# Kernel optimization log

Measured on AMD Instinct MI355X. Metric: run time of the kernel, lower is better.

The kernel has to match this reference:

```python
import jax, jax.numpy as jnp
import numpy as np

DIM = 256
HEADS = 8
GH = GW = 8
NTOK = GH * GW            # 64 tokens per window
NW = 49                   # windows per image (56x56 / 8x8)
BATCH = 64
B_ = BATCH * NW           # 3136
POS_DIM = (DIM // 4) // 4 # 16, DynamicPosBias pos_dim
LBIAS = (2 * GH - 1) * (2 * GW - 1)  # 225 relative offsets
EPS = 1e-5


def _ln(x, g, b):
    m = jnp.mean(x, axis=-1, keepdims=True)
    v = jnp.mean((x - m) ** 2, axis=-1, keepdims=True)
    return (x - m) * jax.lax.rsqrt(v + EPS) * g + b


def _make_buffers():
    # biases: all relative (dh, dw) offsets, shape (LBIAS, 2) float
    h = np.arange(1 - GH, GH)
    w = np.arange(1 - GW, GW)
    biases = np.stack(np.meshgrid(h, w, indexing='ij')).reshape(2, -1).T.astype(np.float32)
    # relative_position_index: (NTOK, NTOK) int32 in [0, LBIAS)
    coords = np.stack(np.meshgrid(np.arange(GH), np.arange(GW), indexing='ij')).reshape(2, -1)
    rel = coords[:, :, None] - coords[:, None, :]
    rel = rel.transpose(1, 2, 0).astype(np.int64)
    rel[..., 0] += GH - 1
    rel[..., 1] += GW - 1
    rel[..., 0] *= 2 * GW - 1
    idx = rel.sum(-1).astype(np.int32)
    return jnp.asarray(biases), jnp.asarray(idx)


def setup_inputs() -> dict:
    key = jax.random.key(0)
    ks = iter(jax.random.split(key, 32))
    def w(shape, s=0.02):
        return jax.random.normal(next(ks), shape, jnp.float32) * s
    biases, rel_idx = _make_buffers()
    return {
        'x': jax.random.normal(next(ks), (B_, NTOK, DIM), jnp.float32),
        'mask': jnp.zeros((NW, NTOK, NTOK), jnp.float32),
        'qkv_w': w((3 * DIM, DIM)), 'qkv_b': jnp.zeros((3 * DIM,), jnp.float32),
        'proj_w': w((DIM, DIM)), 'proj_b': jnp.zeros((DIM,), jnp.float32),
        'pos_proj_w': w((POS_DIM, 2)), 'pos_proj_b': jnp.zeros((POS_DIM,), jnp.float32),
        'ln1_g': jnp.ones((POS_DIM,), jnp.float32), 'ln1_b': jnp.zeros((POS_DIM,), jnp.float32),
        'fc1_w': w((POS_DIM, POS_DIM)), 'fc1_b': jnp.zeros((POS_DIM,), jnp.float32),
        'ln2_g': jnp.ones((POS_DIM,), jnp.float32), 'ln2_b': jnp.zeros((POS_DIM,), jnp.float32),
        'fc2_w': w((POS_DIM, POS_DIM)), 'fc2_b': jnp.zeros((POS_DIM,), jnp.float32),
        'ln3_g': jnp.ones((POS_DIM,), jnp.float32), 'ln3_b': jnp.zeros((POS_DIM,), jnp.float32),
        'fc3_w': w((HEADS, POS_DIM)), 'fc3_b': jnp.zeros((HEADS,), jnp.float32),
        'biases': biases, 'rel_idx': rel_idx,
    }


def _forward(x, mask, qkv_w, qkv_b, proj_w, proj_b,
             pos_proj_w, pos_proj_b, ln1_g, ln1_b, fc1_w, fc1_b,
             ln2_g, ln2_b, fc2_w, fc2_b, ln3_g, ln3_b, fc3_w, fc3_b,
             biases, rel_idx):
    Bw, N, C = x.shape
    hd = C // HEADS
    scale = hd ** -0.5
    qkv = (x @ qkv_w.T + qkv_b).reshape(Bw, N, 3, HEADS, hd)
    qkv = jnp.transpose(qkv, (2, 0, 3, 1, 4))  # (3, B_, H, N, hd)
    q, k, v = qkv[0] * scale, qkv[1], qkv[2]
    attn = jnp.einsum('bhnd,bhmd->bhnm', q, k)  # (B_, H, N, N)
    # DynamicPosBias MLP (residual=False): pos3(pos2(pos1(pos_proj(biases))))
    p = biases @ pos_proj_w.T + pos_proj_b
    p = jax.nn.relu(_ln(p, ln1_g, ln1_b)) @ fc1_w.T + fc1_b
    p = jax.nn.relu(_ln(p, ln2_g, ln2_b)) @ fc2_w.T + fc2_b
    p = jax.nn.relu(_ln(p, ln3_g, ln3_b)) @ fc3_w.T + fc3_b  # (LBIAS, H)
    rpb = jnp.transpose(p[rel_idx], (2, 0, 1))  # gather -> (H, N, N)
    attn = attn + rpb[None]
    nW = mask.shape[0]
    attn = attn.reshape(Bw // nW, nW, HEADS, N, N) + mask[None, :, None]
    attn = jax.nn.softmax(attn.reshape(Bw, HEADS, N, N), axis=-1)
    out = jnp.einsum('bhnm,bhmd->bhnd', attn, v)
    out = jnp.transpose(out, (0, 2, 1, 3)).reshape(Bw, N, C)
    return out @ proj_w.T + proj_b


def reference(x, mask, qkv_w, qkv_b, proj_w, proj_b,
              pos_proj_w, pos_proj_b, ln1_g, ln1_b, fc1_w, fc1_b,
              ln2_g, ln2_b, fc2_w, fc2_b, ln3_g, ln3_b, fc3_w, fc3_b,
              biases, rel_idx):
    return _forward(x, mask, qkv_w, qkv_b, proj_w, proj_b,
                    pos_proj_w, pos_proj_b, ln1_g, ln1_b, fc1_w, fc1_b,
                    ln2_g, ln2_b, fc2_w, fc2_b, ln3_g, ln3_b, fc3_w, fc3_b,
                    biases, rel_idx)
```

## Files before the change

### kernel.cpp

```cpp
#include <hip/hip_runtime.h>

#define NTOKS 64
#define DIMS 256
#define NHEADS 8
#define HDIM 32
#define NWIN 49
#define NBLK 3136

typedef __bf16 bf16x8 __attribute__((ext_vector_type(8)));
typedef float f32x4 __attribute__((ext_vector_type(4)));

__device__ __forceinline__ unsigned short f2bf(float f) {
    union { float f; unsigned u; } c; c.f = f;
    unsigned u = c.u;
    u += 0x7fffu + ((u >> 16) & 1u);
    return (unsigned short)(u >> 16);
}

template<int NOUT>
__device__ __forceinline__ void ln_relu_fc(const float* v, const float* g, const float* bb,
                                           const float* fw, const float* fb, float* o) {
    float m = 0.f;
#pragma unroll
    for (int j = 0; j < 16; ++j) m += v[j];
    m *= (1.f / 16.f);
    float var = 0.f;
#pragma unroll
    for (int j = 0; j < 16; ++j) { float d = v[j] - m; var += d * d; }
    var *= (1.f / 16.f);
    float inv = rsqrtf(var + 1e-5f);
    float t[16];
#pragma unroll
    for (int j = 0; j < 16; ++j) {
        float xx = (v[j] - m) * inv * g[j] + bb[j];
        t[j] = xx > 0.f ? xx : 0.f;
    }
#pragma unroll
    for (int i = 0; i < NOUT; ++i) {
        float ss = fb[i];
#pragma unroll
        for (int j = 0; j < 16; ++j) ss += fw[i * 16 + j] * t[j];
        o[i] = ss;
    }
}

__global__ void prep_kernel(
    const float* __restrict__ qkv_w, const float* __restrict__ qkv_b,
    const float* __restrict__ proj_w, const float* __restrict__ mask,
    const float* __restrict__ pos_proj_w, const float* __restrict__ pos_proj_b,
    const float* __restrict__ ln1_g, const float* __restrict__ ln1_b,
    const float* __restrict__ fc1_w, const float* __restrict__ fc1_b,
    const float* __restrict__ ln2_g, const float* __restrict__ ln2_b,
    const float* __restrict__ fc2_w, const float* __restrict__ fc2_b,
    const float* __restrict__ ln3_g, const float* __restrict__ ln3_b,
    const float* __restrict__ fc3_w, const float* __restrict__ fc3_b,
    const float* __restrict__ biases, const int* __restrict__ rel_idx,
    unsigned short* __restrict__ qkvw_bf, unsigned short* __restrict__ projw_bf,
    float* __restrict__ qkvb_s, float* __restrict__ rpb_perm,
    float* __restrict__ mask_perm)
{
    const int tid = threadIdx.x;
    const int b = blockIdx.x;
    const float SC = 0.17677669529663687f;

    if (b == 0) {
        __shared__ float p_sh[225 * 8];
        if (tid < 225) {
            float bx = biases[2 * tid], by = biases[2 * tid + 1];
            float v[16], u[16];
#pragma unroll
            for (int j = 0; j < 16; ++j)
                v[j] = pos_proj_w[2 * j] * bx + pos_proj_w[2 * j + 1] * by + pos_proj_b[j];
            ln_relu_fc<16>(v, ln1_g, ln1_b, fc1_w, fc1_b, u);
            ln_relu_fc<16>(u, ln2_g, ln2_b, fc2_w, fc2_b, v);
            ln_relu_fc<8>(v, ln3_g, ln3_b, fc3_w, fc3_b, u);
#pragma unroll
            for (int h = 0; h < 8; ++h) p_sh[tid * 8 + h] = u[h];
        }
        __syncthreads();
        for (int e = tid; e < 32768; e += 256) {
            int nt = e & 3, l16 = (e >> 2) & 15, m = (e >> 6) & 63, h = e >> 12;
            rpb_perm[e] = p_sh[rel_idx[m * 64 + nt * 16 + l16] * 8 + h];
        }
    } else {
        const int t0 = (b - 1) * 256 + tid, NTH = 127 * 256;
        for (int e = t0; e < 196608; e += NTH) {
            int j = e & 7, lane = (e >> 3) & 63, kk = (e >> 9) & 7, tile = e >> 12;
            int src = (tile * 16 + (lane & 15)) * 256 + kk * 32 + (lane >> 4) * 8 + j;
            float f = qkv_w[src];
            if (src < 65536) f *= SC;
            qkvw_bf[e] = f2bf(f);
        }
        for (int e = t0; e < 65536; e += NTH) {
            int j = e & 7, lane = (e >> 3) & 63, kk = (e >> 9) & 7, tile = e >> 12;
            int src = (tile * 16 + (lane & 15)) * 256 + kk * 32 + (lane >> 4) * 8 + j;
            projw_bf[e] = f2bf(proj_w[src]);
        }
        for (int e = t0; e < 200704; e += NTH) {
            int nt = e & 3, l16 = (e >> 2) & 15, m = (e >> 6) & 63, w = e >> 12;
            mask_perm[e] = mask[w * 4096 + m * 64 + nt * 16 + l16];
        }
        if (b == 1) {
            for (int e = tid; e < 768; e += 256)
                qkvb_s[e] = qkv_b[e] * (e < 256 ? SC : 1.f);
        }
    }
}

#define XS_OFF 0
#define Q_OFF  16896
#define K_OFF  33792
#define VT_OFF 50688
#define LDS_TOT 69120
#define PS_OFF 0
#define CTX_OFF 0
#define FO_OFF 16896

__global__ __launch_bounds__(1024, 4) void attn_kernel(
    const float* __restrict__ x,
    const unsigned short* __restrict__ qkvw, const float* __restrict__ qkvb,
    const unsigned short* __restrict__ projw, const float* __restrict__ projb,
    const float* __restrict__ rpb_perm, const float* __restrict__ mask_perm,
    float* __restrict__ out)
{
    __shared__ __align__(16) unsigned short lds[LDS_TOT];
    const int tid  = threadIdx.x;
    const int wv   = tid >> 6;
    const int lane = tid & 63;
    const int quad = lane >> 4;
    const int l16  = lane & 15;
    const int blk  = blockIdx.x;
    const int w    = blk % NWIN;
    const f32x4 FZ = {0.f, 0.f, 0.f, 0.f};

    {
        const float4* xv = (const float4*)(x + (size_t)blk * (NTOKS * DIMS));
        for (int i = tid; i < NTOKS * DIMS / 4; i += 1024) {
            float4 f = xv[i];
            int row = i >> 6, c4 = (i & 63) << 2;
            ushort4 u;
            u.x = f2bf(f.x); u.y = f2bf(f.y); u.z = f2bf(f.z); u.w = f2bf(f.w);
            *(ushort4*)&lds[XS_OFF + row * 264 + c4] = u;
        }
    }
    __syncthreads();

    {
        f32x4 acc[4][3];
#pragma unroll
        for (int mt = 0; mt < 4; ++mt)
#pragma unroll
            for (int nt = 0; nt < 3; ++nt) acc[mt][nt] = FZ;
        const unsigned short* wq = qkvw + (size_t)(wv * 3) * 8 * 512;
        for (int kk = 0; kk < 8; ++kk) {
            bf16x8 a[4], bb[3];
#pragma unroll
            for (int mt = 0; mt < 4; ++mt)
                a[mt] = *(const bf16x8*)&lds[XS_OFF + (mt * 16 + l16) * 264 + kk * 32 + quad * 8];
#pragma unroll
            for (int nt = 0; nt < 3; ++nt)
                bb[nt] = *(const bf16x8*)&wq[(nt * 8 + kk) * 512 + lane * 8];
#pragma unroll
            for (int nt = 0; nt < 3; ++nt)
#pragma unroll
                for (int mt = 0; mt < 4; ++mt)
                    acc[mt][nt] = __builtin_amdgcn_mfma_f32_16x16x32_bf16(a[mt], bb[nt], acc[mt][nt], 0, 0, 0);
        }
#pragma unroll
        for (int nt = 0; nt < 3; ++nt) {
            int ob = wv * 48 + nt * 16;
            int o = ob + l16;
            float bias = qkvb[o];
            if (ob < 256) {
#pragma unroll
                for (int mt = 0; mt < 4; ++mt)
#pragma unroll
                    for (int r = 0; r < 4; ++r)
                        lds[Q_OFF + (mt * 16 + quad * 4 + r) * 264 + o] = f2bf(acc[mt][nt][r] + bias);
            } else if (ob < 512) {
                int oo = o - 256;
#pragma unroll
                for (int mt = 0; mt < 4; ++mt)
#pragma unroll
                    for (int r = 0; r < 4; ++r)
                        lds[K_OFF + (mt * 16 + quad * 4 + r) * 264 + oo] = f2bf(acc[mt][nt][r] + bias);
            } else {
                int oo = o - 512;
#pragma unroll
                for (int mt = 0; mt < 4; ++mt) {
                    ushort4 u;
                    u.x = f2bf(acc[mt][nt][0] + bias);
                    u.y = f2bf(acc[mt][nt][1] + bias);
                    u.z = f2bf(acc[mt][nt][2] + bias);
                    u.w = f2bf(acc[mt][nt][3] + bias);
                    *(ushort4*)&lds[VT_OFF + oo * 72 + mt * 16 + quad * 4] = u;
                }
            }
        }
    }
    __syncthreads();

    const int h  = wv >> 1;
    const int hf = wv & 1;
    f32x4 s[2][4];
    {
        bf16x8 aq[2], bk[4];
#pragma unroll
        for (int mt = 0; mt < 2; ++mt)
            aq[mt] = *(const bf16x8*)&lds[Q_OFF + (hf * 32 + mt * 16 + l16) * 264 + h * 32 + quad * 8];
#pragma unroll
        for (int nt = 0; nt < 4; ++nt)
            bk[nt] = *(const bf16x8*)&lds[K_OFF + (nt * 16 + l16) * 264 + h * 32 + quad * 8];
#pragma unroll
        for (int mt = 0; mt < 2; ++mt)
#pragma unroll
            for (int nt = 0; nt < 4; ++nt)
                s[mt][nt] = __builtin_amdgcn_mfma_f32_16x16x32_bf16(aq[mt], bk[nt], FZ, 0, 0, 0);
    }
    {
        const f32x4* rp4 = (const f32x4*)rpb_perm;
        const f32x4* mk4 = (const f32x4*)mask_perm;
#pragma unroll
        for (int mt = 0; mt < 2; ++mt)
#pragma unroll
            for (int r = 0; r < 4; ++r) {
                int m = hf * 32 + mt * 16 + quad * 4 + r;
                f32x4 rv = rp4[(h * 64 + m) * 16 + l16];
                f32x4 mv = mk4[(w * 64 + m) * 16 + l16];
#pragma unroll
                for (int nt = 0; nt < 4; ++nt)
                    s[mt][nt][r] += rv[nt] + mv[nt];
            }
    }
#pragma unroll
    for (int mt = 0; mt < 2; ++mt)
#pragma unroll
        for (int r = 0; r < 4; ++r) {
            float mx = fmaxf(fmaxf(s[mt][0][r], s[mt][1][r]), fmaxf(s[mt][2][r], s[mt][3][r]));
            mx = fmaxf(mx, __shfl_xor(mx, 1));
            mx = fmaxf(mx, __shfl_xor(mx, 2));
            mx = fmaxf(mx, __shfl_xor(mx, 4));
            mx = fmaxf(mx, __shfl_xor(mx, 8));
            float sum = 0.f;
#pragma unroll
            for (int nt = 0; nt < 4; ++nt) {
                float e = __expf(s[mt][nt][r] - mx);
                s[mt][nt][r] = e; sum += e;
            }
            sum += __shfl_xor(sum, 1);
            sum += __shfl_xor(sum, 2);
            sum += __shfl_xor(sum, 4);
            sum += __shfl_xor(sum, 8);
            float inv = 1.0f / sum;
#pragma unroll
            for (int nt = 0; nt < 4; ++nt) s[mt][nt][r] *= inv;
        }
    __syncthreads();

#pragma unroll
    for (int mt = 0; mt < 2; ++mt)
#pragma unroll
        for (int r = 0; r < 4; ++r) {
            int m = hf * 32 + mt * 16 + quad * 4 + r;
#pragma unroll
            for (int nt = 0; nt < 4; ++nt)
                lds[PS_OFF + h * 4608 + m * 72 + nt * 16 + l16] = f2bf(s[mt][nt][r]);
        }
    __syncthreads();

    f32x4 ov[2][2];
#pragma unroll
    for (int mt = 0; mt < 2; ++mt)
#pragma unroll
        for (int nt = 0; nt < 2; ++nt) ov[mt][nt] = FZ;
#pragma unroll
    for (int ks = 0; ks < 2; ++ks) {
        bf16x8 ap[2], bv[2];
#pragma unroll
        for (int mt = 0; mt < 2; ++mt)
            ap[mt] = *(const bf16x8*)&lds[PS_OFF + h * 4608 + (hf * 32 + mt * 16 + l16) * 72 + ks * 32 + quad * 8];
#pragma unroll
        for (int nt = 0; nt < 2; ++nt)
            bv[nt] = *(const bf16x8*)&lds[VT_OFF + (h * 32 + nt * 16 + l16) * 72 + ks * 32 + quad * 8];
#pragma unroll
        for (int mt = 0; mt < 2; ++mt)
#pragma unroll
            for (int nt = 0; nt < 2; ++nt)
                ov[mt][nt] = __builtin_amdgcn_mfma_f32_16x16x32_bf16(ap[mt], bv[nt], ov[mt][nt], 0, 0, 0);
    }
    __syncthreads();

#pragma unroll
    for (int mt = 0; mt < 2; ++mt)
#pragma unroll
        for (int r = 0; r < 4; ++r) {
            int t = hf * 32 + mt * 16 + quad * 4 + r;
#pragma unroll
            for (int nt = 0; nt < 2; ++nt)
                lds[CTX_OFF + t * 264 + h * 32 + nt * 16 + l16] = f2bf(ov[mt][nt][r]);
        }
    __syncthreads();

    {
        f32x4 accC[4];
#pragma unroll
        for (int mt = 0; mt < 4; ++mt) accC[mt] = FZ;
        const unsigned short* pw = projw + (size_t)wv * 8 * 512;
        for (int kk = 0; kk < 8; ++kk) {
            bf16x8 a[4];
#pragma unroll
            for (int mt = 0; mt < 4; ++mt)
                a[mt] = *(const bf16x8*)&lds[CTX_OFF + (mt * 16 + l16) * 264 + kk * 32 + quad * 8];
            bf16x8 bb = *(const bf16x8*)&pw[kk * 512 + lane * 8];
#pragma unroll
            for (int mt = 0; mt < 4; ++mt)
                accC[mt] = __builtin_amdgcn_mfma_f32_16x16x32_bf16(a[mt], bb, accC[mt], 0, 0, 0);
        }
        float* fo = (float*)&lds[FO_OFF];
        int o = wv * 16 + l16;
        float pb = projb[o];
#pragma unroll
        for (int mt = 0; mt < 4; ++mt)
#pragma unroll
            for (int r = 0; r < 4; ++r)
                fo[(mt * 16 + quad * 4 + r) * 260 + o] = accC[mt][r] + pb;
    }
    __syncthreads();
    {
        float* ob = out + (size_t)blk * (NTOKS * DIMS);
        const float* fo = (const float*)&lds[FO_OFF];
        for (int i = tid; i < NTOKS * DIMS / 4; i += 1024) {
            int row = i >> 6, c4 = (i & 63) << 2;
            float4 v = *(const float4*)&fo[row * 260 + c4];
            *(float4*)&ob[row * 256 + c4] = v;
        }
    }
}

extern "C" void kernel_launch(void* const* d_in, const int* in_sizes, int n_in,
                              void* d_out, int out_size, void* d_ws, size_t ws_size,
                              hipStream_t stream) {
    const float* x          = (const float*)d_in[0];
    const float* mask       = (const float*)d_in[1];
    const float* qkv_w      = (const float*)d_in[2];
    const float* qkv_b      = (const float*)d_in[3];
    const float* proj_w     = (const float*)d_in[4];
    const float* proj_b     = (const float*)d_in[5];
    const float* pos_proj_w = (const float*)d_in[6];
    const float* pos_proj_b = (const float*)d_in[7];
    const float* ln1_g      = (const float*)d_in[8];
    const float* ln1_b      = (const float*)d_in[9];
    const float* fc1_w      = (const float*)d_in[10];
    const float* fc1_b      = (const float*)d_in[11];
    const float* ln2_g      = (const float*)d_in[12];
    const float* ln2_b      = (const float*)d_in[13];
    const float* fc2_w      = (const float*)d_in[14];
    const float* fc2_b      = (const float*)d_in[15];
    const float* ln3_g      = (const float*)d_in[16];
    const float* ln3_b      = (const float*)d_in[17];
    const float* fc3_w      = (const float*)d_in[18];
    const float* fc3_b      = (const float*)d_in[19];
    const float* biases     = (const float*)d_in[20];
    const int*   rel_idx    = (const int*)d_in[21];
    float* out = (float*)d_out;

    char* ws = (char*)d_ws;
    unsigned short* qkvw_bf  = (unsigned short*)(ws);
    unsigned short* projw_bf = (unsigned short*)(ws + 393216);
    float* qkvb_s    = (float*)(ws + 524288);
    float* rpb_perm  = (float*)(ws + 528384);
    float* mask_perm = (float*)(ws + 659456);

    prep_kernel<<<dim3(128), dim3(256), 0, stream>>>(
        qkv_w, qkv_b, proj_w, mask, pos_proj_w, pos_proj_b,
        ln1_g, ln1_b, fc1_w, fc1_b, ln2_g, ln2_b, fc2_w, fc2_b,
        ln3_g, ln3_b, fc3_w, fc3_b, biases, rel_idx,
        qkvw_bf, projw_bf, qkvb_s, rpb_perm, mask_perm);

    attn_kernel<<<dim3(NBLK), dim3(1024), 0, stream>>>(
        x, qkvw_bf, qkvb_s, projw_bf, proj_b, rpb_perm, mask_perm, out);
}
```

Measured before the change: 604.8 us.

## Restructure attention to one wave per head with register-resident Q/K/V/P

The attention kernel is rebuilt so each of 8 waves owns one head. Each wave computes its own Q, K and V slices straight into MFMA register fragments (Q/K computed transposed), runs the scores, softmax and PV in registers, and only stages the context through an XOR-swizzled LDS buffer before the output projection. The output is written directly to global memory rather than through an LDS staging pass. The rpb/mask permutations in the prep kernel are changed to match the new transposed score layout. This removes several LDS round-trips and barriers and shrinks LDS use. In exchange, register pressure per wave rises, blocks are 512 threads, and the global stores are 4-byte scattered writes instead of float4.

```diff
diff --git a/kernel.cpp b/kernel.cpp
--- a/kernel.cpp
+++ b/kernel.cpp
@@ -3,11 +3,11 @@
 #define NTOKS 64
 #define DIMS 256
 #define NHEADS 8
-#define HDIM 32
 #define NWIN 49
 #define NBLK 3136
 
 typedef __bf16 bf16x8 __attribute__((ext_vector_type(8)));
+typedef __bf16 bf16x4 __attribute__((ext_vector_type(4)));
 typedef float f32x4 __attribute__((ext_vector_type(4)));
 
 __device__ __forceinline__ unsigned short f2bf(float f) {
@@ -15,6 +15,15 @@
     unsigned u = c.u;
     u += 0x7fffu + ((u >> 16) & 1u);
     return (unsigned short)(u >> 16);
+}
+
+__device__ __forceinline__ bf16x8 pack8(f32x4 a, f32x4 b) {
+    bf16x8 r;
+    r[0] = (__bf16)a[0]; r[1] = (__bf16)a[1];
+    r[2] = (__bf16)a[2]; r[3] = (__bf16)a[3];
+    r[4] = (__bf16)b[0]; r[5] = (__bf16)b[1];
+    r[6] = (__bf16)b[2]; r[7] = (__bf16)b[3];
+    return r;
 }
 
 template<int NOUT>
@@ -79,8 +88,9 @@
         }
         __syncthreads();
         for (int e = tid; e < 32768; e += 256) {
-            int nt = e & 3, l16 = (e >> 2) & 15, m = (e >> 6) & 63, h = e >> 12;
-            rpb_perm[e] = p_sh[rel_idx[m * 64 + nt * 16 + l16] * 8 + h];
+            int r = e & 3, q = (e >> 2) & 63, qd = (e >> 8) & 3, kt = (e >> 10) & 3, h = e >> 12;
+            int key = kt * 16 + qd * 4 + r;
+            rpb_perm[e] = p_sh[rel_idx[q * 64 + key] * 8 + h];
         }
     } else {
         const int t0 = (b - 1) * 256 + tid, NTH = 127 * 256;
@@ -97,8 +107,9 @@
             projw_bf[e] = f2bf(proj_w[src]);
         }
         for (int e = t0; e < 200704; e += NTH) {
-            int nt = e & 3, l16 = (e >> 2) & 15, m = (e >> 6) & 63, w = e >> 12;
-            mask_perm[e] = mask[w * 4096 + m * 64 + nt * 16 + l16];
+            int r = e & 3, q = (e >> 2) & 63, qd = (e >> 8) & 3, kt = (e >> 10) & 3, w = e >> 12;
+            int key = kt * 16 + qd * 4 + r;
+            mask_perm[e] = mask[w * 4096 + q * 64 + key];
         }
         if (b == 1) {
             for (int e = tid; e < 768; e += 256)
@@ -107,234 +118,234 @@
     }
 }
 
-#define XS_OFF 0
-#define Q_OFF  16896
-#define K_OFF  33792
-#define VT_OFF 50688
-#define LDS_TOT 69120
-#define PS_OFF 0
-#define CTX_OFF 0
-#define FO_OFF 16896
-
-__global__ __launch_bounds__(1024, 4) void attn_kernel(
+__global__ __launch_bounds__(512, 4) void attn_kernel(
     const float* __restrict__ x,
     const unsigned short* __restrict__ qkvw, const float* __restrict__ qkvb,
     const unsigned short* __restrict__ projw, const float* __restrict__ projb,
     const float* __restrict__ rpb_perm, const float* __restrict__ mask_perm,
     float* __restrict__ out)
 {
-    __shared__ __align__(16) unsigned short lds[LDS_TOT];
+    __shared__ __align__(16) char ldsb[65536];
     const int tid  = threadIdx.x;
-    const int wv   = tid >> 6;
+    const int h    = tid >> 6;
     const int lane = tid & 63;
     const int quad = lane >> 4;
     const int l16  = lane & 15;
+    const int sw   = (l16 & 7) << 4;
     const int blk  = blockIdx.x;
     const int w    = blk % NWIN;
     const f32x4 FZ = {0.f, 0.f, 0.f, 0.f};
 
     {
         const float4* xv = (const float4*)(x + (size_t)blk * (NTOKS * DIMS));
-        for (int i = tid; i < NTOKS * DIMS / 4; i += 1024) {
+#pragma unroll
+        for (int it = 0; it < 8; ++it) {
+            int i = tid + it * 512;
             float4 f = xv[i];
-            int row = i >> 6, c4 = (i & 63) << 2;
-            ushort4 u;
-            u.x = f2bf(f.x); u.y = f2bf(f.y); u.z = f2bf(f.z); u.w = f2bf(f.w);
-            *(ushort4*)&lds[XS_OFF + row * 264 + c4] = u;
+            int row = i >> 6;
+            int colb = (i & 63) << 3;
+            bf16x4 hv;
+            hv[0] = (__bf16)f.x; hv[1] = (__bf16)f.y;
+            hv[2] = (__bf16)f.z; hv[3] = (__bf16)f.w;
+            *(bf16x4*)(ldsb + row * 512 + (colb ^ ((row & 7) << 4))) = hv;
         }
     }
     __syncthreads();
 
-    {
-        f32x4 acc[4][3];
+    const int xbase = l16 * 512;
+#define XFRAG(t, kk) (*(const bf16x8*)(ldsb + (t) * 8192 + xbase + ((((kk) * 64) + quad * 16) ^ sw)))
+#define CFRAG(t, kk) (*(const bf16x8*)(ldsb + 32768 + (t) * 8192 + xbase + ((((kk) * 64) + quad * 16) ^ sw)))
+
+    f32x4 qa[2][4], ka[2][4];
+#pragma unroll
+    for (int mt = 0; mt < 2; ++mt)
+#pragma unroll
+        for (int nt = 0; nt < 4; ++nt) { qa[mt][nt] = FZ; ka[mt][nt] = FZ; }
+    {
+        const unsigned short* pQ = qkvw + (size_t)((2 * h) * 8) * 512 + lane * 8;
+        const unsigned short* pK = qkvw + (size_t)((16 + 2 * h) * 8) * 512 + lane * 8;
+#pragma unroll 2
+        for (int kk = 0; kk < 8; ++kk) {
+            bf16x8 xb[4];
+#pragma unroll
+            for (int nt = 0; nt < 4; ++nt) xb[nt] = XFRAG(nt, kk);
+            bf16x8 wq[2], wk[2];
+#pragma unroll
+            for (int mt = 0; mt < 2; ++mt) {
+                wq[mt] = *(const bf16x8*)&pQ[(mt * 8 + kk) * 512];
+                wk[mt] = *(const bf16x8*)&pK[(mt * 8 + kk) * 512];
+            }
+#pragma unroll
+            for (int mt = 0; mt < 2; ++mt)
+#pragma unroll
+                for (int nt = 0; nt < 4; ++nt) {
+                    qa[mt][nt] = __builtin_amdgcn_mfma_f32_16x16x32_bf16(wq[mt], xb[nt], qa[mt][nt], 0, 0, 0);
+                    ka[mt][nt] = __builtin_amdgcn_mfma_f32_16x16x32_bf16(wk[mt], xb[nt], ka[mt][nt], 0, 0, 0);
+                }
+        }
+    }
+#pragma unroll
+    for (int mt = 0; mt < 2; ++mt) {
+        f32x4 qb = *(const f32x4*)&qkvb[h * 32 + mt * 16 + quad * 4];
+        f32x4 kb = *(const f32x4*)&qkvb[256 + h * 32 + mt * 16 + quad * 4];
+#pragma unroll
+        for (int nt = 0; nt < 4; ++nt) {
+#pragma unroll
+            for (int r = 0; r < 4; ++r) { qa[mt][nt][r] += qb[r]; ka[mt][nt][r] += kb[r]; }
+        }
+    }
+    bf16x8 Qp[4], Kp[4];
+#pragma unroll
+    for (int t = 0; t < 4; ++t) {
+        Qp[t] = pack8(qa[0][t], qa[1][t]);
+        Kp[t] = pack8(ka[0][t], ka[1][t]);
+    }
+
+    f32x4 s[4][4];
+    {
+        const f32x4* rp4 = (const f32x4*)rpb_perm + ((h * 16 + quad) * 64 + l16);
+        const f32x4* mp4 = (const f32x4*)mask_perm + ((w * 16 + quad) * 64 + l16);
+#pragma unroll
+        for (int kt = 0; kt < 4; ++kt)
+#pragma unroll
+            for (int qt = 0; qt < 4; ++qt) {
+                f32x4 rv = rp4[kt * 256 + qt * 16];
+                f32x4 mv = mp4[kt * 256 + qt * 16];
+                s[kt][qt] = rv + mv;
+            }
+#pragma unroll
+        for (int kt = 0; kt < 4; ++kt)
+#pragma unroll
+            for (int qt = 0; qt < 4; ++qt)
+                s[kt][qt] = __builtin_amdgcn_mfma_f32_16x16x32_bf16(Kp[kt], Qp[qt], s[kt][qt], 0, 0, 0);
+    }
+
+#pragma unroll
+    for (int qt = 0; qt < 4; ++qt) {
+        float mx = s[0][qt][0];
+#pragma unroll
+        for (int kt = 0; kt < 4; ++kt)
+#pragma unroll
+            for (int r = 0; r < 4; ++r) mx = fmaxf(mx, s[kt][qt][r]);
+        mx = fmaxf(mx, __shfl_xor(mx, 16));
+        mx = fmaxf(mx, __shfl_xor(mx, 32));
+        float sum = 0.f;
+#pragma unroll
+        for (int kt = 0; kt < 4; ++kt)
+#pragma unroll
+            for (int r = 0; r < 4; ++r) {
+                float e = __expf(s[kt][qt][r] - mx);
+                s[kt][qt][r] = e; sum += e;
+            }
+        sum += __shfl_xor(sum, 16);
+        sum += __shfl_xor(sum, 32);
+        float inv = 1.0f / sum;
+#pragma unroll
+        for (int kt = 0; kt < 4; ++kt)
+#pragma unroll
+            for (int r = 0; r < 4; ++r) s[kt][qt][r] *= inv;
+    }
+    bf16x8 Pp[4][2];
+#pragma unroll
+    for (int qt = 0; qt < 4; ++qt)
+#pragma unroll
+        for (int ks = 0; ks < 2; ++ks)
+            Pp[qt][ks] = pack8(s[2 * ks][qt], s[2 * ks + 1][qt]);
+
+    f32x4 va[4][2];
+#pragma unroll
+    for (int mt = 0; mt < 4; ++mt)
+#pragma unroll
+        for (int nt = 0; nt < 2; ++nt) va[mt][nt] = FZ;
+    {
+        const unsigned short* pV = qkvw + (size_t)((32 + 2 * h) * 8) * 512 + lane * 8;
+#pragma unroll 2
+        for (int kk = 0; kk < 8; ++kk) {
+            bf16x8 xa[4];
+#pragma unroll
+            for (int mt = 0; mt < 4; ++mt) xa[mt] = XFRAG(mt, kk);
+            bf16x8 wv[2];
+#pragma unroll
+            for (int nt = 0; nt < 2; ++nt) wv[nt] = *(const bf16x8*)&pV[(nt * 8 + kk) * 512];
+#pragma unroll
+            for (int mt = 0; mt < 4; ++mt)
+#pragma unroll
+                for (int nt = 0; nt < 2; ++nt)
+                    va[mt][nt] = __builtin_amdgcn_mfma_f32_16x16x32_bf16(xa[mt], wv[nt], va[mt][nt], 0, 0, 0);
+        }
+        float vb0 = qkvb[512 + h * 32 + l16];
+        float vb1 = qkvb[512 + h * 32 + 16 + l16];
 #pragma unroll
         for (int mt = 0; mt < 4; ++mt)
 #pragma unroll
-            for (int nt = 0; nt < 3; ++nt) acc[mt][nt] = FZ;
-        const unsigned short* wq = qkvw + (size_t)(wv * 3) * 8 * 512;
-        for (int kk = 0; kk < 8; ++kk) {
-            bf16x8 a[4], bb[3];
-#pragma unroll
-            for (int mt = 0; mt < 4; ++mt)
-                a[mt] = *(const bf16x8*)&lds[XS_OFF + (mt * 16 + l16) * 264 + kk * 32 + quad * 8];
-#pragma unroll
-            for (int nt = 0; nt < 3; ++nt)
-                bb[nt] = *(const bf16x8*)&wq[(nt * 8 + kk) * 512 + lane * 8];
-#pragma unroll
-            for (int nt = 0; nt < 3; ++nt)
-#pragma unroll
-                for (int mt = 0; mt < 4; ++mt)
-                    acc[mt][nt] = __builtin_amdgcn_mfma_f32_16x16x32_bf16(a[mt], bb[nt], acc[mt][nt], 0, 0, 0);
-        }
-#pragma unroll
-        for (int nt = 0; nt < 3; ++nt) {
-            int ob = wv * 48 + nt * 16;
-            int o = ob + l16;
-            float bias = qkvb[o];
-            if (ob < 256) {
-#pragma unroll
-                for (int mt = 0; mt < 4; ++mt)
-#pragma unroll
-                    for (int r = 0; r < 4; ++r)
-                        lds[Q_OFF + (mt * 16 + quad * 4 + r) * 264 + o] = f2bf(acc[mt][nt][r] + bias);
-            } else if (ob < 512) {
-                int oo = o - 256;
-#pragma unroll
-                for (int mt = 0; mt < 4; ++mt)
-#pragma unroll
-                    for (int r = 0; r < 4; ++r)
-                        lds[K_OFF + (mt * 16 + quad * 4 + r) * 264 + oo] = f2bf(acc[mt][nt][r] + bias);
-            } else {
-                int oo = o - 512;
-#pragma unroll
-                for (int mt = 0; mt < 4; ++mt) {
-                    ushort4 u;
-                    u.x = f2bf(acc[mt][nt][0] + bias);
-                    u.y = f2bf(acc[mt][nt][1] + bias);
-                    u.z = f2bf(acc[mt][nt][2] + bias);
-                    u.w = f2bf(acc[mt][nt][3] + bias);
-                    *(ushort4*)&lds[VT_OFF + oo * 72 + mt * 16 + quad * 4] = u;
-                }
-            }
-        }
+            for (int r = 0; r < 4; ++r) { va[mt][0][r] += vb0; va[mt][1][r] += vb1; }
+    }
+    bf16x8 Vp[2][2];
+#pragma unroll
+    for (int ks = 0; ks < 2; ++ks)
+#pragma unroll
+        for (int nt = 0; nt < 2; ++nt)
+            Vp[ks][nt] = pack8(va[2 * ks][nt], va[2 * ks + 1][nt]);
+
+    f32x4 o[4][2];
+#pragma unroll
+    for (int qt = 0; qt < 4; ++qt)
+#pragma unroll
+        for (int nt = 0; nt < 2; ++nt) {
+            f32x4 a0 = __builtin_amdgcn_mfma_f32_16x16x32_bf16(Pp[qt][0], Vp[0][nt], FZ, 0, 0, 0);
+            o[qt][nt] = __builtin_amdgcn_mfma_f32_16x16x32_bf16(Pp[qt][1], Vp[1][nt], a0, 0, 0, 0);
+        }
+
+    {
+        const int chb = 2 * (h * 32 + l16);
+#pragma unroll
+        for (int qt = 0; qt < 4; ++qt)
+#pragma unroll
+            for (int r = 0; r < 4; ++r) {
+                int row = qt * 16 + quad * 4 + r;
+                int rsw = (row & 7) << 4;
+#pragma unroll
+                for (int nt = 0; nt < 2; ++nt)
+                    *(__bf16*)(ldsb + 32768 + row * 512 + ((chb + 32 * nt) ^ rsw)) = (__bf16)o[qt][nt][r];
+            }
     }
     __syncthreads();
 
-    const int h  = wv >> 1;
-    const int hf = wv & 1;
-    f32x4 s[2][4];
-    {
-        bf16x8 aq[2], bk[4];
-#pragma unroll
-        for (int mt = 0; mt < 2; ++mt)
-            aq[mt] = *(const bf16x8*)&lds[Q_OFF + (hf * 32 + mt * 16 + l16) * 264 + h * 32 + quad * 8];
-#pragma unroll
-        for (int nt = 0; nt < 4; ++nt)
-            bk[nt] = *(const bf16x8*)&lds[K_OFF + (nt * 16 + l16) * 264 + h * 32 + quad * 8];
-#pragma unroll
-        for (int mt = 0; mt < 2; ++mt)
-#pragma unroll
-            for (int nt = 0; nt < 4; ++nt)
-                s[mt][nt] = __builtin_amdgcn_mfma_f32_16x16x32_bf16(aq[mt], bk[nt], FZ, 0, 0, 0);
-    }
-    {
-        const f32x4* rp4 = (const f32x4*)rpb_perm;
-        const f32x4* mk4 = (const f32x4*)mask_perm;
-#pragma unroll
-        for (int mt = 0; mt < 2; ++mt)
-#pragma unroll
-            for (int r = 0; r < 4; ++r) {
-                int m = hf * 32 + mt * 16 + quad * 4 + r;
-                f32x4 rv = rp4[(h * 64 + m) * 16 + l16];
-                f32x4 mv = mk4[(w * 64 + m) * 16 + l16];
-#pragma unroll
-                for (int nt = 0; nt < 4; ++nt)
-                    s[mt][nt][r] += rv[nt] + mv[nt];
-            }
-    }
-#pragma unroll
-    for (int mt = 0; mt < 2; ++mt)
-#pragma unroll
-        for (int r = 0; r < 4; ++r) {
-            float mx = fmaxf(fmaxf(s[mt][0][r], s[mt][1][r]), fmaxf(s[mt][2][r], s[mt][3][r]));
-            mx = fmaxf(mx, __shfl_xor(mx, 1));
-            mx = fmaxf(mx, __shfl_xor(mx, 2));
-            mx = fmaxf(mx, __shfl_xor(mx, 4));
-            mx = fmaxf(mx, __shfl_xor(mx, 8));
-            float sum = 0.f;
-#pragma unroll
-            for (int nt = 0; nt < 4; ++nt) {
-                float e = __expf(s[mt][nt][r] - mx);
-                s[mt][nt][r] = e; sum += e;
-            }
-            sum += __shfl_xor(sum, 1);
-            sum += __shfl_xor(sum, 2);
-            sum += __shfl_xor(sum, 4);
-            sum += __shfl_xor(sum, 8);
-            float inv = 1.0f / sum;
-#pragma unroll
-            for (int nt = 0; nt < 4; ++nt) s[mt][nt][r] *= inv;
-        }
-    __syncthreads();
-
-#pragma unroll
-    for (int mt = 0; mt < 2; ++mt)
-#pragma unroll
-        for (int r = 0; r < 4; ++r) {
-            int m = hf * 32 + mt * 16 + quad * 4 + r;
-#pragma unroll
-            for (int nt = 0; nt < 4; ++nt)
-                lds[PS_OFF + h * 4608 + m * 72 + nt * 16 + l16] = f2bf(s[mt][nt][r]);
-        }
-    __syncthreads();
-
-    f32x4 ov[2][2];
-#pragma unroll
-    for (int mt = 0; mt < 2; ++mt)
-#pragma unroll
-        for (int nt = 0; nt < 2; ++nt) ov[mt][nt] = FZ;
-#pragma unroll
-    for (int ks = 0; ks < 2; ++ks) {
-        bf16x8 ap[2], bv[2];
-#pragma unroll
-        for (int mt = 0; mt < 2; ++mt)
-            ap[mt] = *(const bf16x8*)&lds[PS_OFF + h * 4608 + (hf * 32 + mt * 16 + l16) * 72 + ks * 32 + quad * 8];
-#pragma unroll
-        for (int nt = 0; nt < 2; ++nt)
-            bv[nt] = *(const bf16x8*)&lds[VT_OFF + (h * 32 + nt * 16 + l16) * 72 + ks * 32 + quad * 8];
-#pragma unroll
-        for (int mt = 0; mt < 2; ++mt)
-#pragma unroll
-            for (int nt = 0; nt < 2; ++nt)
-                ov[mt][nt] = __builtin_amdgcn_mfma_f32_16x16x32_bf16(ap[mt], bv[nt], ov[mt][nt], 0, 0, 0);
-    }
-    __syncthreads();
-
-#pragma unroll
-    for (int mt = 0; mt < 2; ++mt)
-#pragma unroll
-        for (int r = 0; r < 4; ++r) {
-            int t = hf * 32 + mt * 16 + quad * 4 + r;
-#pragma unroll
-            for (int nt = 0; nt < 2; ++nt)
-                lds[CTX_OFF + t * 264 + h * 32 + nt * 16 + l16] = f2bf(ov[mt][nt][r]);
-        }
-    __syncthreads();
-
-    {
-        f32x4 accC[4];
-#pragma unroll
-        for (int mt = 0; mt < 4; ++mt) accC[mt] = FZ;
-        const unsigned short* pw = projw + (size_t)wv * 8 * 512;
+    {
+        f32x4 c_[4][2];
+#pragma unroll
+        for (int mt = 0; mt < 4; ++mt)
+#pragma unroll
+            for (int nt = 0; nt < 2; ++nt) c_[mt][nt] = FZ;
+        const unsigned short* pP = projw + (size_t)((2 * h) * 8) * 512 + lane * 8;
+#pragma unroll 2
         for (int kk = 0; kk < 8; ++kk) {
             bf16x8 a[4];
 #pragma unroll
+            for (int mt = 0; mt < 4; ++mt) a[mt] = CFRAG(mt, kk);
+            bf16x8 bwp[2];
+#pragma unroll
+            for (int nt = 0; nt < 2; ++nt) bwp[nt] = *(const bf16x8*)&pP[(nt * 8 + kk) * 512];
+#pragma unroll
             for (int mt = 0; mt < 4; ++mt)
-                a[mt] = *(const bf16x8*)&lds[CTX_OFF + (mt * 16 + l16) * 264 + kk * 32 + quad * 8];
-            bf16x8 bb = *(const bf16x8*)&pw[kk * 512 + lane * 8];
-#pragma unroll
-            for (int mt = 0; mt < 4; ++mt)
-                accC[mt] = __builtin_amdgcn_mfma_f32_16x16x32_bf16(a[mt], bb, accC[mt], 0, 0, 0);
-        }
-        float* fo = (float*)&lds[FO_OFF];
-        int o = wv * 16 + l16;
-        float pb = projb[o];
+#pragma unroll
+                for (int nt = 0; nt < 2; ++nt)
+                    c_[mt][nt] = __builtin_amdgcn_mfma_f32_16x16x32_bf16(a[mt], bwp[nt], c_[mt][nt], 0, 0, 0);
+        }
+        float pb0 = projb[h * 32 + l16];
+        float pb1 = projb[h * 32 + 16 + l16];
+        float* ob = out + (size_t)blk * (NTOKS * DIMS) + h * 32 + l16;
 #pragma unroll
         for (int mt = 0; mt < 4; ++mt)
 #pragma unroll
-            for (int r = 0; r < 4; ++r)
-                fo[(mt * 16 + quad * 4 + r) * 260 + o] = accC[mt][r] + pb;
-    }
-    __syncthreads();
-    {
-        float* ob = out + (size_t)blk * (NTOKS * DIMS);
-        const float* fo = (const float*)&lds[FO_OFF];
-        for (int i = tid; i < NTOKS * DIMS / 4; i += 1024) {
-            int row = i >> 6, c4 = (i & 63) << 2;
-            float4 v = *(const float4*)&fo[row * 260 + c4];
-            *(float4*)&ob[row * 256 + c4] = v;
-        }
-    }
+            for (int r = 0; r < 4; ++r) {
+                int row = mt * 16 + quad * 4 + r;
+                ob[row * 256]      = c_[mt][0][r] + pb0;
+                ob[row * 256 + 16] = c_[mt][1][r] + pb1;
+            }
+    }
+#undef XFRAG
+#undef CFRAG
 }
 
 extern "C" void kernel_launch(void* const* d_in, const int* in_sizes, int n_in,
@@ -377,6 +388,6 @@
         ln3_g, ln3_b, fc3_w, fc3_b, biases, rel_idx,
         qkvw_bf, projw_bf, qkvb_s, rpb_perm, mask_perm);
 
-    attn_kernel<<<dim3(NBLK), dim3(1024), 0, stream>>>(
+    attn_kernel<<<dim3(NBLK), dim3(512), 0, stream>>>(
         x, qkvw_bf, qkvb_s, projw_bf, proj_b, rpb_perm, mask_perm, out);
 }
```

New measurement: 517.5 us. 1.17x faster.
